# Kernel optimization log

Hardware: AMD Instinct MI355X
Metric: run time of the kernel (lower is better)

The kernel has to match this reference:

```python
import jax, jax.numpy as jnp
import numpy as np

E = 500_000
H = 128
L = 3
N = 10_000


def setup_inputs() -> dict:
    key = jax.random.key(0)
    ks = jax.random.split(key, 9)
    s = 1.0 / np.sqrt(H)  # torch Linear default init scale
    return {
        "m": jax.random.normal(ks[0], (E, H), dtype=jnp.float32),
        "edge_index": jax.random.randint(ks[1], (2, E), 0, N, dtype=jnp.int64),
        "n_nodes": N,
        "W1": jax.random.uniform(ks[2], (L, H, H), jnp.float32, -s, s),
        "b1": jax.random.uniform(ks[3], (L, H), jnp.float32, -s, s),
        "W2": jax.random.uniform(ks[4], (L, H, H), jnp.float32, -s, s),
        "b2": jax.random.uniform(ks[5], (L, H), jnp.float32, -s, s),
        "Wlin": jax.random.uniform(ks[6], (H, H), jnp.float32, -s, s),
        "blin": jax.random.uniform(ks[7], (H,), jnp.float32, -s, s),
    }


def reference(m, edge_index, n_nodes, W1, b1, W2, b2, Wlin, blin):
    act = jax.nn.silu
    # Pre-activation residual stack: x + lin2(act(lin1(act(x))))
    for i in range(W1.shape[0]):
        h = act(m) @ W1[i].T + b1[i]
        m = m + (act(h) @ W2[i].T + b2[i])
    m = act(m @ Wlin.T + blin)  # [E, H]
    # scatter-add edge messages into target nodes (edge_index[1])
    out = jax.ops.segment_sum(m, edge_index[1], num_segments=n_nodes)  # [N, H]
    return out
```

## Files before the change

### kernel.cpp

```cpp
#include <hip/hip_runtime.h>
#include <hip/hip_bf16.h>

#define HDIM 128
#define NSTAGE 7
#define CHUNK_LOG 13
#define CHUNK (1 << CHUNK_LOG)

typedef __bf16 bf16x8 __attribute__((ext_vector_type(8)));
typedef __bf16 bf16x4 __attribute__((ext_vector_type(4)));
typedef float floatx16 __attribute__((ext_vector_type(16)));
typedef float floatx4 __attribute__((ext_vector_type(4)));

__device__ __forceinline__ float silu_f(float x) {
    return x * __builtin_amdgcn_rcpf(1.0f + __expf(-x));
}

__global__ void convert_weights(const float* __restrict__ W1,
                                const float* __restrict__ W2,
                                const float* __restrict__ Wlin,
                                __bf16* __restrict__ dst) {
    int idx = blockIdx.x * blockDim.x + threadIdx.x;
    if (idx >= NSTAGE * HDIM * HDIM) return;
    int s    = idx >> 14;
    int rem  = idx & 16383;
    int mrow = rem >> 7;
    int k    = rem & 127;
    const float* src;
    if (s == 6) src = Wlin;
    else {
        int l = s >> 1;
        src = ((s & 1) ? W2 : W1) + l * HDIM * HDIM;
    }
    float v = src[mrow * HDIM + k];
    int dsti = (s << 14) + (mrow << 7) + ((((k >> 3) ^ (mrow & 7)) << 3) | (k & 7));
    dst[dsti] = (__bf16)v;
}

__global__ __launch_bounds__(1024) void hist_rank_kernel(
    const int* __restrict__ tgt,
    unsigned short* __restrict__ rank,
    int* __restrict__ hb,
    int E, int N)
{
    __shared__ int lh[10240];
    for (int i = threadIdx.x; i < N; i += 1024) lh[i] = 0;
    __syncthreads();
    int ebase = blockIdx.x << CHUNK_LOG;
    int eend  = min(ebase + CHUNK, E);
    for (int e = ebase + (int)threadIdx.x; e < eend; e += 1024) {
        int node = tgt[e];
        int r = atomicAdd(&lh[node], 1);
        rank[e] = (unsigned short)r;
    }
    __syncthreads();
    int* row = hb + (size_t)blockIdx.x * N;
    for (int i = threadIdx.x; i < N; i += 1024) row[i] = lh[i];
}

__global__ void colsum_kernel(const int* __restrict__ hb, int* __restrict__ tot,
                              int nblk, int N) {
    int n = blockIdx.x * blockDim.x + threadIdx.x;
    if (n >= N) return;
    int s = 0;
    for (int b = 0; b < nblk; ++b) s += hb[(size_t)b * N + n];
    tot[n] = s;
}

__global__ __launch_bounds__(1024) void scan_kernel(const int* __restrict__ hist,
                                                    int* __restrict__ cursor, int N) {
    __shared__ int part[1024];
    int t = threadIdx.x;
    int per = (N + 1023) >> 10;
    int lo = t * per, hi = min(lo + per, N);
    int s = 0;
    for (int i = lo; i < hi; ++i) s += hist[i];
    part[t] = s;
    __syncthreads();
    for (int d = 1; d < 1024; d <<= 1) {
        int v = (t >= d) ? part[t - d] : 0;
        __syncthreads();
        part[t] += v;
        __syncthreads();
    }
    int off = (t == 0) ? 0 : part[t - 1];
    for (int i = lo; i < hi; ++i) { cursor[i] = off; off += hist[i]; }
}

__global__ void offsets_kernel(int* __restrict__ hb, const int* __restrict__ base,
                               int nblk, int N) {
    int n = blockIdx.x * blockDim.x + threadIdx.x;
    if (n >= N) return;
    int run = base[n];
    for (int b = 0; b < nblk; ++b) {
        size_t idx = (size_t)b * N + n;
        int c = hb[idx];
        hb[idx] = run;
        run += c;
    }
}

__global__ void emit_perm_kernel(const int* __restrict__ tgt,
                                 const unsigned short* __restrict__ rank,
                                 const int* __restrict__ hb,
                                 int* __restrict__ perm, int* __restrict__ snode,
                                 int E, int N) {
    int e = blockIdx.x * blockDim.x + threadIdx.x;
    if (e >= E) return;
    int node = tgt[e];
    int b = e >> CHUNK_LOG;
    int pos = hb[(size_t)b * N + node] + (int)rank[e];
    perm[pos] = e;
    snode[pos] = node;
}

__global__ __launch_bounds__(256, 2) void fused_mlp_scatter(
    const float* __restrict__ m,
    const int* __restrict__ perm,
    const int* __restrict__ snode,
    const __bf16* __restrict__ wmats,
    const float* __restrict__ b1,
    const float* __restrict__ b2,
    const float* __restrict__ blin,
    float* __restrict__ out,
    int E, int ntiles)
{
    __shared__ __align__(16) char smem[67584];
    __bf16* wlds   = (__bf16*)smem;
    __bf16* actAll = (__bf16*)(smem + 32768);
    float*  ybuf   = (float*)smem;

    const int tid  = threadIdx.x;
    const int w    = tid >> 6;
    const int lane = tid & 63;
    const int l31  = lane & 31;
    const int half = lane >> 5;

    const int tile    = blockIdx.x * 4 + w;
    const bool activeW = (tile < ntiles);
    const int pos = tile * 32 + l31;
    const bool evalid = activeW && (pos < E);

    int eidx = 0, mynode = 0;
    if (evalid) { eidx = perm[pos]; mynode = snode[pos]; }

    floatx4 X[4][4];
    floatx16 acc[4];
    bf16x8 wpre[8];
    __bf16* actw = actAll + (w * 32 + l31) * 136;

    #define ACT_OFF(f) (((((((f) >> 4) + l31) & 7)) << 4) | ((f) & 15))

    #pragma unroll
    for (int i = 0; i < 8; ++i)
        wpre[i] = *(const bf16x8*)(wmats + i * 2048 + tid * 8);

    if (activeW) {
        const float* mrow = m + (size_t)eidx * HDIM;
        #pragma unroll
        for (int mb = 0; mb < 4; ++mb)
            #pragma unroll
            for (int q = 0; q < 4; ++q) {
                int f0 = mb * 32 + q * 8 + half * 4;
                X[mb][q] = *(const floatx4*)(mrow + f0);
            }
        #pragma unroll
        for (int mb = 0; mb < 4; ++mb)
            #pragma unroll
            for (int q = 0; q < 4; ++q) {
                int f0 = mb * 32 + q * 8 + half * 4;
                bf16x4 v;
                for (int j = 0; j < 4; ++j) v[j] = (__bf16)silu_f(X[mb][q][j]);
                *(bf16x4*)(actw + ACT_OFF(f0)) = v;
            }
    }

    #pragma unroll
    for (int s = 0; s < NSTAGE; ++s) {
        __syncthreads();
        #pragma unroll
        for (int i = 0; i < 8; ++i)
            *(bf16x8*)(&wlds[i * 2048 + tid * 8]) = wpre[i];
        __syncthreads();
        if (s < NSTAGE - 1) {
            const __bf16* wsrc = wmats + ((s + 1) << 14);
            #pragma unroll
            for (int i = 0; i < 8; ++i)
                wpre[i] = *(const bf16x8*)(wsrc + i * 2048 + tid * 8);
        }
        if (!activeW) continue;

        #pragma unroll
        for (int mb = 0; mb < 4; ++mb)
            for (int r = 0; r < 16; ++r) acc[mb][r] = 0.0f;

        #pragma unroll
        for (int ks = 0; ks < 8; ++ks) {
            bf16x8 bfrag = *(const bf16x8*)(actw + ((((ks + l31) & 7) << 4) + half * 8));
            int krow = ks * 2 + half;
            #pragma unroll
            for (int mb = 0; mb < 4; ++mb) {
                int mr = mb * 32 + l31;
                bf16x8 afrag = *(const bf16x8*)(&wlds[(mr << 7) + ((krow ^ (mr & 7)) << 3)]);
                acc[mb] = __builtin_amdgcn_mfma_f32_32x32x16_bf16(afrag, bfrag, acc[mb], 0, 0, 0);
            }
        }

        if (s == 6) {
            #pragma unroll
            for (int mb = 0; mb < 4; ++mb)
                #pragma unroll
                for (int q = 0; q < 4; ++q) {
                    int f0 = mb * 32 + q * 8 + half * 4;
                    floatx4 bv = *(const floatx4*)(blin + f0);
                    for (int j = 0; j < 4; ++j)
                        acc[mb][q * 4 + j] = silu_f(acc[mb][q * 4 + j] + bv[j]);
                }
        } else if ((s & 1) == 0) {
            const float* bias = b1 + (s >> 1) * HDIM;
            #pragma unroll
            for (int mb = 0; mb < 4; ++mb)
                #pragma unroll
                for (int q = 0; q < 4; ++q) {
                    int f0 = mb * 32 + q * 8 + half * 4;
                    floatx4 bv = *(const floatx4*)(bias + f0);
                    bf16x4 hv;
                    for (int j = 0; j < 4; ++j)
                        hv[j] = (__bf16)silu_f(acc[mb][q * 4 + j] + bv[j]);
                    *(bf16x4*)(actw + ACT_OFF(f0)) = hv;
                }
        } else {
            const float* bias = b2 + (s >> 1) * HDIM;
            #pragma unroll
            for (int mb = 0; mb < 4; ++mb)
                #pragma unroll
                for (int q = 0; q < 4; ++q) {
                    int f0 = mb * 32 + q * 8 + half * 4;
                    floatx4 bv = *(const floatx4*)(bias + f0);
                    bf16x4 xv;
                    for (int j = 0; j < 4; ++j) {
                        float nx = X[mb][q][j] + acc[mb][q * 4 + j] + bv[j];
                        X[mb][q][j] = nx;
                        xv[j] = (__bf16)((s == 5) ? nx : silu_f(nx));
                    }
                    *(bf16x4*)(actw + ACT_OFF(f0)) = xv;
                }
        }
    }

    __syncthreads();
    if (activeW) {
        float* yrow = ybuf + (w * 32 + l31) * 132;
        #pragma unroll
        for (int mb = 0; mb < 4; ++mb)
            #pragma unroll
            for (int q = 0; q < 4; ++q) {
                int f0 = mb * 32 + q * 8 + half * 4;
                floatx4 v;
                for (int j = 0; j < 4; ++j) v[j] = acc[mb][q * 4 + j];
                *(floatx4*)(yrow + f0) = v;
            }
        const float* yb = ybuf + w * 32 * 132;
        const int ebase = tile * 32;
        const int cnt = min(32, E - ebase);
        int cur = __builtin_amdgcn_readlane(mynode, 0);
        float a0 = 0.f, a1 = 0.f;
        for (int e = 0; e < cnt; ++e) {
            int node = __builtin_amdgcn_readlane(mynode, e);
            if (node != cur) {
                float* op = out + (size_t)cur * HDIM;
                unsafeAtomicAdd(op + lane, a0);
                unsafeAtomicAdd(op + 64 + lane, a1);
                cur = node; a0 = 0.f; a1 = 0.f;
            }
            a0 += yb[e * 132 + lane];
            a1 += yb[e * 132 + 64 + lane];
        }
        float* op = out + (size_t)cur * HDIM;
        unsafeAtomicAdd(op + lane, a0);
        unsafeAtomicAdd(op + 64 + lane, a1);
    }
    #undef ACT_OFF
}

extern "C" void kernel_launch(void* const* d_in, const int* in_sizes, int n_in,
                              void* d_out, int out_size, void* d_ws, size_t ws_size,
                              hipStream_t stream) {
    const float* m      = (const float*)d_in[0];
    const int* edge_idx = (const int*)d_in[1];
    const float* W1     = (const float*)d_in[3];
    const float* b1     = (const float*)d_in[4];
    const float* W2     = (const float*)d_in[5];
    const float* b2     = (const float*)d_in[6];
    const float* Wlin   = (const float*)d_in[7];
    const float* blin   = (const float*)d_in[8];

    int E = in_sizes[0] / HDIM;
    int N = out_size / HDIM;
    const int* tgt = edge_idx + E;

    int nblk = (E + CHUNK - 1) >> CHUNK_LOG;

    char* ws = (char*)d_ws;
    size_t off = 0;
    auto align_up = [](size_t v) { return (v + 255) & ~(size_t)255; };

    __bf16* wbf = (__bf16*)(ws + off);
    off = align_up(off + (size_t)NSTAGE * HDIM * HDIM * sizeof(__bf16));
    unsigned short* rank = (unsigned short*)(ws + off);
    off = align_up(off + (size_t)E * sizeof(unsigned short));
    int* hb = (int*)(ws + off);
    off = align_up(off + (size_t)nblk * N * sizeof(int));
    int* tot = (int*)(ws + off);
    off = align_up(off + (size_t)N * sizeof(int));
    int* base = (int*)(ws + off);
    off = align_up(off + (size_t)N * sizeof(int));
    int* perm = (int*)(ws + off);
    off = align_up(off + (size_t)E * sizeof(int));
    int* snode = (int*)(ws + off);
    off = align_up(off + (size_t)E * sizeof(int));

    hipMemsetAsync(d_out, 0, (size_t)out_size * sizeof(float), stream);

    convert_weights<<<(NSTAGE * HDIM * HDIM + 255) / 256, 256, 0, stream>>>(W1, W2, Wlin, wbf);

    hist_rank_kernel<<<nblk, 1024, 0, stream>>>(tgt, rank, hb, E, N);
    colsum_kernel<<<(N + 255) / 256, 256, 0, stream>>>(hb, tot, nblk, N);
    scan_kernel<<<1, 1024, 0, stream>>>(tot, base, N);
    offsets_kernel<<<(N + 255) / 256, 256, 0, stream>>>(hb, base, nblk, N);
    emit_perm_kernel<<<(E + 255) / 256, 256, 0, stream>>>(tgt, rank, hb, perm, snode, E, N);

    int ntiles  = (E + 31) / 32;
    int nblocks = (ntiles + 3) / 4;
    fused_mlp_scatter<<<nblocks, 256, 0, stream>>>(m, perm, snode, wbf, b1, b2, blin,
                                                   (float*)d_out, E, ntiles);
}
```

Before: 649.7 us.

## Keep MFMA activation fragments in registers via lane shuffles, shrink LDS for occupancy

Activations are no longer staged through a per-row LDS buffer. The MFMA B fragments are built directly in registers by packing bf16 pairs and swapping halves across the wave with shfl_xor. This lets shared memory drop from about 66KB to 36KB, and the launch bounds are raised to 3 blocks per CU. Bias is folded into the accumulator initialisation, and the final scatter is done in two 64-column passes so the smaller LDS buffer suffices. The extra bw[8][4] register array may cause register pressure or spills at the higher occupancy target.

```diff
diff --git a/kernel.cpp b/kernel.cpp
--- a/kernel.cpp
+++ b/kernel.cpp
@@ -7,12 +7,25 @@
 #define CHUNK (1 << CHUNK_LOG)
 
 typedef __bf16 bf16x8 __attribute__((ext_vector_type(8)));
-typedef __bf16 bf16x4 __attribute__((ext_vector_type(4)));
+typedef __bf16 bf16x2 __attribute__((ext_vector_type(2)));
 typedef float floatx16 __attribute__((ext_vector_type(16)));
 typedef float floatx4 __attribute__((ext_vector_type(4)));
+typedef int intx4 __attribute__((ext_vector_type(4)));
 
 __device__ __forceinline__ float silu_f(float x) {
     return x * __builtin_amdgcn_rcpf(1.0f + __expf(-x));
+}
+
+__device__ __forceinline__ int pack2(float a, float b) {
+    bf16x2 h;
+    h[0] = (__bf16)a;
+    h[1] = (__bf16)b;
+    return __builtin_bit_cast(int, h);
+}
+
+__device__ __forceinline__ bf16x8 frag_from(int w0, int w1, int w2, int w3) {
+    intx4 v; v[0] = w0; v[1] = w1; v[2] = w2; v[3] = w3;
+    return __builtin_bit_cast(bf16x8, v);
 }
 
 __global__ void convert_weights(const float* __restrict__ W1,
@@ -113,7 +126,7 @@
     snode[pos] = node;
 }
 
-__global__ __launch_bounds__(256, 2) void fused_mlp_scatter(
+__global__ __launch_bounds__(256, 3) void fused_mlp_scatter(
     const float* __restrict__ m,
     const int* __restrict__ perm,
     const int* __restrict__ snode,
@@ -124,10 +137,9 @@
     float* __restrict__ out,
     int E, int ntiles)
 {
-    __shared__ __align__(16) char smem[67584];
-    __bf16* wlds   = (__bf16*)smem;
-    __bf16* actAll = (__bf16*)(smem + 32768);
-    float*  ybuf   = (float*)smem;
+    __shared__ __align__(16) char smem[36864];
+    __bf16* wlds = (__bf16*)smem;
+    float*  ybuf = (float*)smem;
 
     const int tid  = threadIdx.x;
     const int w    = tid >> 6;
@@ -146,9 +158,17 @@
     floatx4 X[4][4];
     floatx16 acc[4];
     bf16x8 wpre[8];
-    __bf16* actw = actAll + (w * 32 + l31) * 136;
-
-    #define ACT_OFF(f) (((((((f) >> 4) + l31) & 7)) << 4) | ((f) & 15))
+    int bw[8][4];
+
+    #define BUILD_BW(KS, VA0,VA1,VA2,VA3, VB0,VB1,VB2,VB3) do {              \
+        int A0_ = pack2((VA0), (VA1)); int A1_ = pack2((VA2), (VA3));        \
+        int B0_ = pack2((VB0), (VB1)); int B1_ = pack2((VB2), (VB3));        \
+        int N0_ = half ? A0_ : B0_;  int N1_ = half ? A1_ : B1_;             \
+        int S0_ = __shfl_xor(N0_, 32, 64);                                   \
+        int S1_ = __shfl_xor(N1_, 32, 64);                                   \
+        bw[KS][0] = half ? S0_ : A0_;  bw[KS][1] = half ? S1_ : A1_;         \
+        bw[KS][2] = half ? B0_ : S0_;  bw[KS][3] = half ? B1_ : S1_;         \
+    } while (0)
 
     #pragma unroll
     for (int i = 0; i < 8; ++i)
@@ -164,14 +184,14 @@
                 X[mb][q] = *(const floatx4*)(mrow + f0);
             }
         #pragma unroll
-        for (int mb = 0; mb < 4; ++mb)
-            #pragma unroll
-            for (int q = 0; q < 4; ++q) {
-                int f0 = mb * 32 + q * 8 + half * 4;
-                bf16x4 v;
-                for (int j = 0; j < 4; ++j) v[j] = (__bf16)silu_f(X[mb][q][j]);
-                *(bf16x4*)(actw + ACT_OFF(f0)) = v;
-            }
+        for (int ks = 0; ks < 8; ++ks) {
+            int mb = ks >> 1, qa = (ks & 1) * 2, qb = qa + 1;
+            BUILD_BW(ks,
+                silu_f(X[mb][qa][0]), silu_f(X[mb][qa][1]),
+                silu_f(X[mb][qa][2]), silu_f(X[mb][qa][3]),
+                silu_f(X[mb][qb][0]), silu_f(X[mb][qb][1]),
+                silu_f(X[mb][qb][2]), silu_f(X[mb][qb][3]));
+        }
     }
 
     #pragma unroll
@@ -189,13 +209,23 @@
         }
         if (!activeW) continue;
 
-        #pragma unroll
-        for (int mb = 0; mb < 4; ++mb)
-            for (int r = 0; r < 16; ++r) acc[mb][r] = 0.0f;
+        {
+            const float* bias = (s == 6) ? blin
+                              : ((s & 1) ? b2 + (s >> 1) * HDIM
+                                         : b1 + (s >> 1) * HDIM);
+            #pragma unroll
+            for (int mb = 0; mb < 4; ++mb)
+                #pragma unroll
+                for (int q = 0; q < 4; ++q) {
+                    floatx4 bv = *(const floatx4*)(bias + mb * 32 + q * 8 + half * 4);
+                    #pragma unroll
+                    for (int j = 0; j < 4; ++j) acc[mb][q * 4 + j] = bv[j];
+                }
+        }
 
         #pragma unroll
         for (int ks = 0; ks < 8; ++ks) {
-            bf16x8 bfrag = *(const bf16x8*)(actw + ((((ks + l31) & 7) << 4) + half * 8));
+            bf16x8 bfrag = frag_from(bw[ks][0], bw[ks][1], bw[ks][2], bw[ks][3]);
             int krow = ks * 2 + half;
             #pragma unroll
             for (int mb = 0; mb < 4; ++mb) {
@@ -209,77 +239,74 @@
             #pragma unroll
             for (int mb = 0; mb < 4; ++mb)
                 #pragma unroll
-                for (int q = 0; q < 4; ++q) {
-                    int f0 = mb * 32 + q * 8 + half * 4;
-                    floatx4 bv = *(const floatx4*)(blin + f0);
-                    for (int j = 0; j < 4; ++j)
-                        acc[mb][q * 4 + j] = silu_f(acc[mb][q * 4 + j] + bv[j]);
-                }
+                for (int r = 0; r < 16; ++r)
+                    acc[mb][r] = silu_f(acc[mb][r]);
         } else if ((s & 1) == 0) {
-            const float* bias = b1 + (s >> 1) * HDIM;
-            #pragma unroll
-            for (int mb = 0; mb < 4; ++mb)
-                #pragma unroll
-                for (int q = 0; q < 4; ++q) {
-                    int f0 = mb * 32 + q * 8 + half * 4;
-                    floatx4 bv = *(const floatx4*)(bias + f0);
-                    bf16x4 hv;
-                    for (int j = 0; j < 4; ++j)
-                        hv[j] = (__bf16)silu_f(acc[mb][q * 4 + j] + bv[j]);
-                    *(bf16x4*)(actw + ACT_OFF(f0)) = hv;
-                }
+            #pragma unroll
+            for (int ks = 0; ks < 8; ++ks) {
+                int mb = ks >> 1, qa = (ks & 1) * 2, qb = qa + 1;
+                BUILD_BW(ks,
+                    silu_f(acc[mb][qa * 4 + 0]), silu_f(acc[mb][qa * 4 + 1]),
+                    silu_f(acc[mb][qa * 4 + 2]), silu_f(acc[mb][qa * 4 + 3]),
+                    silu_f(acc[mb][qb * 4 + 0]), silu_f(acc[mb][qb * 4 + 1]),
+                    silu_f(acc[mb][qb * 4 + 2]), silu_f(acc[mb][qb * 4 + 3]));
+            }
         } else {
-            const float* bias = b2 + (s >> 1) * HDIM;
-            #pragma unroll
-            for (int mb = 0; mb < 4; ++mb)
-                #pragma unroll
-                for (int q = 0; q < 4; ++q) {
-                    int f0 = mb * 32 + q * 8 + half * 4;
-                    floatx4 bv = *(const floatx4*)(bias + f0);
-                    bf16x4 xv;
-                    for (int j = 0; j < 4; ++j) {
-                        float nx = X[mb][q][j] + acc[mb][q * 4 + j] + bv[j];
-                        X[mb][q][j] = nx;
-                        xv[j] = (__bf16)((s == 5) ? nx : silu_f(nx));
-                    }
-                    *(bf16x4*)(actw + ACT_OFF(f0)) = xv;
-                }
+            #pragma unroll
+            for (int ks = 0; ks < 8; ++ks) {
+                int mb = ks >> 1, qa = (ks & 1) * 2, qb = qa + 1;
+                float va[4], vb[4];
+                #pragma unroll
+                for (int j = 0; j < 4; ++j) {
+                    float nx = X[mb][qa][j] + acc[mb][qa * 4 + j];
+                    X[mb][qa][j] = nx;
+                    va[j] = (s == 5) ? nx : silu_f(nx);
+                }
+                #pragma unroll
+                for (int j = 0; j < 4; ++j) {
+                    float nx = X[mb][qb][j] + acc[mb][qb * 4 + j];
+                    X[mb][qb][j] = nx;
+                    vb[j] = (s == 5) ? nx : silu_f(nx);
+                }
+                BUILD_BW(ks, va[0], va[1], va[2], va[3],
+                             vb[0], vb[1], vb[2], vb[3]);
+            }
         }
     }
 
     __syncthreads();
     if (activeW) {
-        float* yrow = ybuf + (w * 32 + l31) * 132;
-        #pragma unroll
-        for (int mb = 0; mb < 4; ++mb)
-            #pragma unroll
-            for (int q = 0; q < 4; ++q) {
-                int f0 = mb * 32 + q * 8 + half * 4;
-                floatx4 v;
-                for (int j = 0; j < 4; ++j) v[j] = acc[mb][q * 4 + j];
-                *(floatx4*)(yrow + f0) = v;
-            }
-        const float* yb = ybuf + w * 32 * 132;
         const int ebase = tile * 32;
         const int cnt = min(32, E - ebase);
-        int cur = __builtin_amdgcn_readlane(mynode, 0);
-        float a0 = 0.f, a1 = 0.f;
-        for (int e = 0; e < cnt; ++e) {
-            int node = __builtin_amdgcn_readlane(mynode, e);
-            if (node != cur) {
-                float* op = out + (size_t)cur * HDIM;
-                unsafeAtomicAdd(op + lane, a0);
-                unsafeAtomicAdd(op + 64 + lane, a1);
-                cur = node; a0 = 0.f; a1 = 0.f;
-            }
-            a0 += yb[e * 132 + lane];
-            a1 += yb[e * 132 + 64 + lane];
-        }
-        float* op = out + (size_t)cur * HDIM;
-        unsafeAtomicAdd(op + lane, a0);
-        unsafeAtomicAdd(op + 64 + lane, a1);
-    }
-    #undef ACT_OFF
+        float* yrow = ybuf + (w * 32 + l31) * 72;
+        const float* yb = ybuf + w * 32 * 72;
+        #pragma unroll
+        for (int p = 0; p < 2; ++p) {
+            #pragma unroll
+            for (int mbh = 0; mbh < 2; ++mbh) {
+                int mb = 2 * p + mbh;
+                #pragma unroll
+                for (int q = 0; q < 4; ++q) {
+                    int f0 = mbh * 32 + q * 8 + half * 4;
+                    floatx4 v;
+                    for (int j = 0; j < 4; ++j) v[j] = acc[mb][q * 4 + j];
+                    *(floatx4*)(yrow + f0) = v;
+                }
+            }
+            int cur = __builtin_amdgcn_readlane(mynode, 0);
+            float a0 = 0.f;
+            for (int e = 0; e < cnt; ++e) {
+                int node = __builtin_amdgcn_readlane(mynode, e);
+                if (node != cur) {
+                    unsafeAtomicAdd(out + (size_t)cur * HDIM + p * 64 + lane, a0);
+                    cur = node; a0 = 0.f;
+                }
+                a0 += yb[e * 72 + lane];
+            }
+            unsafeAtomicAdd(out + (size_t)cur * HDIM + p * 64 + lane, a0);
+        }
+    }
+    #undef BUILD_BW
 }
 
 extern "C" void kernel_launch(void* const* d_in, const int* in_sizes, int n_in,
```

New measurement: 762.9 us. 17.4% more time.
